# Performance work log

Measured on AMD Instinct MI355X. Metric: run time of the kernel, lower is better.

## Reference

```python
import jax, jax.numpy as jnp
import numpy as np

B, H, W, C = 2, 128, 256, 64
NHEAD, K, HIDDEN = 2, 9, 256
HD = C // NHEAD


def _layer_norm(x, g, b, eps=1e-5):
    m = jnp.mean(x, -1, keepdims=True)
    v = jnp.mean((x - m) ** 2, -1, keepdims=True)
    return (x - m) * jax.lax.rsqrt(v + eps) * g + b


def _grid_sample(img, gx, gy):
    """Bilinear grid_sample, zeros padding, align_corners=False.
    img: (N, Ch, Hh, Ww); gx, gy: (N, P) normalized coords in [-1, 1].
    Returns (N, Ch, P)."""
    N, Ch, Hh, Ww = img.shape
    ix = (gx + 1.0) * (Ww * 0.5) - 0.5
    iy = (gy + 1.0) * (Hh * 0.5) - 0.5
    x0 = jnp.floor(ix)
    y0 = jnp.floor(iy)
    flat = img.reshape(N, Ch, Hh * Ww)

    def gather(xi, yi):
        valid = (xi >= 0) & (xi <= Ww - 1) & (yi >= 0) & (yi <= Hh - 1)
        xc = jnp.clip(xi, 0, Ww - 1).astype(jnp.int32)
        yc = jnp.clip(yi, 0, Hh - 1).astype(jnp.int32)
        vals = jnp.take_along_axis(flat, (yc * Ww + xc)[:, None, :], axis=2)
        return vals * valid[:, None, :].astype(img.dtype)

    wx1 = ix - x0
    wy1 = iy - y0
    return (gather(x0, y0) * ((1 - wx1) * (1 - wy1))[:, None, :]
            + gather(x0 + 1, y0) * (wx1 * (1 - wy1))[:, None, :]
            + gather(x0, y0 + 1) * ((1 - wx1) * wy1)[:, None, :]
            + gather(x0 + 1, y0 + 1) * (wx1 * wy1)[:, None, :])


def setup_inputs() -> dict:
    key = jax.random.key(0)
    ks = jax.random.split(key, 16)
    s = 0.02
    inp = {}
    inp['x'] = jax.random.normal(ks[0], (B, H * W, C), jnp.float32)
    # spherical-style reference points: 3x3 pixel neighborhood per query, normalized coords
    ys = (np.arange(H) + 0.5) / H * 2 - 1
    xs = (np.arange(W) + 0.5) / W * 2 - 1
    gy, gx = np.meshgrid(ys, xs, indexing='ij')
    dy, dx = np.meshgrid(np.array([-1, 0, 1]), np.array([-1, 0, 1]), indexing='ij')
    offs = np.stack([dx.ravel() * 2.0 / W, dy.ravel() * 2.0 / H], -1)  # (9,2) in (x,y)
    ref = np.stack([gx, gy], -1)[:, :, None, :] + offs[None, None]     # (H,W,9,2)
    inp['ref_point'] = jnp.asarray(np.broadcast_to(ref, (B, H, W, K, 2)).copy(), jnp.float32)
    # norm1 / norm2
    inp['g1'] = jnp.ones((C,), jnp.float32); inp['be1'] = jnp.zeros((C,), jnp.float32)
    inp['g2'] = jnp.ones((C,), jnp.float32); inp['be2'] = jnp.zeros((C,), jnp.float32)
    # deformable attention projections
    inp['Woff'] = jax.random.normal(ks[1], (C, NHEAD * K * 2), jnp.float32) * s
    inp['boff'] = jnp.zeros((NHEAD * K * 2,), jnp.float32)
    inp['Wa'] = jax.random.normal(ks[2], (C, NHEAD * K), jnp.float32) * s
    inp['ba'] = jnp.zeros((NHEAD * K,), jnp.float32)
    inp['Wv'] = jax.random.normal(ks[3], (C, C), jnp.float32) * s
    inp['bv'] = jnp.zeros((C,), jnp.float32)
    inp['Wo'] = jax.random.normal(ks[4], (C, C), jnp.float32) * s
    inp['bo'] = jnp.zeros((C,), jnp.float32)
    # LeFF
    inp['W1'] = jax.random.normal(ks[5], (C, HIDDEN), jnp.float32) * s
    inp['c1'] = jnp.zeros((HIDDEN,), jnp.float32)
    inp['Wdw'] = jax.random.normal(ks[6], (HIDDEN, 1, 3, 3), jnp.float32) * s
    inp['bdw'] = jnp.zeros((HIDDEN,), jnp.float32)
    inp['W2'] = jax.random.normal(ks[7], (HIDDEN, C), jnp.float32) * s
    inp['c2'] = jnp.zeros((C,), jnp.float32)
    return inp


def reference(x, ref_point, g1, be1, g2, be2, Woff, boff, Wa, ba, Wv, bv, Wo, bo,
              W1, c1, Wdw, bdw, W2, c2):
    # ---- norm1 + deformable k=9 point-sampling self-attention ----
    h = _layer_norm(x, g1, be1).reshape(B, H, W, C)
    off = (h @ Woff + boff).reshape(B, H, W, NHEAD, K, 2)
    attn = jax.nn.softmax((h @ Wa + ba).reshape(B, H, W, NHEAD, K), axis=-1)
    v = (h @ Wv + bv).reshape(B, H, W, NHEAD, HD)
    v = v.transpose(0, 3, 4, 1, 2).reshape(B * NHEAD, HD, H, W)
    loc = ref_point[:, :, :, None] + off                     # (B,H,W,NHEAD,K,2)
    loc = loc.transpose(0, 3, 1, 2, 4, 5).reshape(B * NHEAD, H * W * K, 2)
    samp = _grid_sample(v, loc[..., 0], loc[..., 1])          # (B*NHEAD, HD, H*W*K)
    samp = samp.reshape(B, NHEAD, HD, H, W, K)
    out = jnp.einsum('bnchwk,bhwnk->bhwnc', samp, attn).reshape(B, H, W, C)
    out = (out @ Wo + bo).reshape(B, H * W, C)
    x = x + out                                               # residual
    # ---- norm2 + LeFF (linear -> circular-pad depthwise 3x3 -> linear) ----
    y = _layer_norm(x, g2, be2)
    y = jax.nn.gelu(y @ W1 + c1, approximate=False)
    y = y.reshape(B, H, W, HIDDEN).transpose(0, 3, 1, 2)      # (B,HIDDEN,H,W)
    y = jnp.pad(y, ((0, 0), (0, 0), (0, 0), (1, 1)), mode='wrap')   # circular in width
    y = jnp.pad(y, ((0, 0), (0, 0), (1, 1), (0, 0)))                # zeros in height
    y = jax.lax.conv_general_dilated(y, Wdw, (1, 1), 'VALID',
                                     dimension_numbers=('NCHW', 'OIHW', 'NCHW'),
                                     feature_group_count=HIDDEN)
    y = jax.nn.gelu(y + bdw[None, :, None, None], approximate=False)
    y = y.transpose(0, 2, 3, 1).reshape(B, H * W, HIDDEN)
    y = y @ W2 + c2
    return x + y
```

## Files before the change

kernel.cpp:

```cpp
#include <hip/hip_runtime.h>
#include <math.h>

#define Bq 2
#define Hq 128
#define Wq 256
#define Cq 64
#define HIDq 256
#define HWq (Hq * Wq)
#define NTOK (Bq * HWq)

#define TOKA 64
#define TOKB 64
#define TOKC 64
#define PIXD 32

typedef __attribute__((ext_vector_type(8))) short short8v;
typedef __attribute__((ext_vector_type(4))) float f32x4v;
typedef __attribute__((ext_vector_type(4))) unsigned short ushort4v;
typedef __attribute__((ext_vector_type(4))) unsigned int uint4v;

__device__ inline float gelu_exact(float x) {
    return 0.5f * x * (1.0f + erff(x * 0.70710678118654752440f));
}

__device__ inline unsigned short f2bf(float f) {
    unsigned int u = __float_as_uint(f);
    u += 0x7FFFu + ((u >> 16) & 1u);
    return (unsigned short)(u >> 16);
}

__device__ inline float bf2f(unsigned short u) {
    return __uint_as_float(((unsigned int)u) << 16);
}

__global__ __launch_bounds__(256) void kPrep(
    const float* __restrict__ W1, const float* __restrict__ W2,
    const float* __restrict__ Wv, const float* __restrict__ Woff, const float* __restrict__ Wa,
    unsigned short* __restrict__ w1t, unsigned short* __restrict__ w2t,
    unsigned short* __restrict__ wct)
{
    const int p = blockIdx.x * 256 + threadIdx.x;
    if (p < 8192) {
        const int c = p >> 5, k2 = p & 31;
        const unsigned int pk = (unsigned int)f2bf(W1[(size_t)(2 * k2) * 256 + c])
                              | ((unsigned int)f2bf(W1[(size_t)(2 * k2 + 1) * 256 + c]) << 16);
        ((unsigned int*)w1t)[c * 32 + k2] = pk;
    } else if (p < 16384) {
        const int q = p - 8192;
        const int c = q >> 7, k2 = q & 127;
        const unsigned int pk = (unsigned int)f2bf(W2[(size_t)(2 * k2) * 64 + c])
                              | ((unsigned int)f2bf(W2[(size_t)(2 * k2 + 1) * 64 + c]) << 16);
        ((unsigned int*)w2t)[c * 128 + k2] = pk;
    } else {
        const int q = p - 16384;
        const int c = q >> 5, k2 = q & 31;
        float w0 = 0.0f, w1 = 0.0f;
        if (c < 64)       { w0 = Wv[(size_t)(2 * k2) * 64 + c];          w1 = Wv[(size_t)(2 * k2 + 1) * 64 + c]; }
        else if (c < 100) { w0 = Woff[(size_t)(2 * k2) * 36 + (c - 64)]; w1 = Woff[(size_t)(2 * k2 + 1) * 36 + (c - 64)]; }
        else if (c < 118) { w0 = Wa[(size_t)(2 * k2) * 18 + (c - 100)];  w1 = Wa[(size_t)(2 * k2 + 1) * 18 + (c - 100)]; }
        const unsigned int pk = (unsigned int)f2bf(w0) | ((unsigned int)f2bf(w1) << 16);
        ((unsigned int*)wct)[c * 32 + k2] = pk;
    }
}

__device__ inline void ln_to_bf16_lds(
    const float* __restrict__ xsrc, const float* __restrict__ g, const float* __restrict__ be,
    int tok0, int t, unsigned short* __restrict__ hdst)
{
    const int tok = t >> 2, part = t & 3;
    const int chb = part * 16;
    const float* xp = xsrc + (size_t)(tok0 + tok) * 64 + chb;
    const float4 v0 = ((const float4*)xp)[0];
    const float4 v1 = ((const float4*)xp)[1];
    const float4 v2 = ((const float4*)xp)[2];
    const float4 v3 = ((const float4*)xp)[3];
    float s = ((v0.x + v0.y) + (v0.z + v0.w)) + ((v1.x + v1.y) + (v1.z + v1.w))
            + ((v2.x + v2.y) + (v2.z + v2.w)) + ((v3.x + v3.y) + (v3.z + v3.w));
    float s2 = 0.0f;
    s2 = fmaf(v0.x, v0.x, s2); s2 = fmaf(v0.y, v0.y, s2);
    s2 = fmaf(v0.z, v0.z, s2); s2 = fmaf(v0.w, v0.w, s2);
    s2 = fmaf(v1.x, v1.x, s2); s2 = fmaf(v1.y, v1.y, s2);
    s2 = fmaf(v1.z, v1.z, s2); s2 = fmaf(v1.w, v1.w, s2);
    s2 = fmaf(v2.x, v2.x, s2); s2 = fmaf(v2.y, v2.y, s2);
    s2 = fmaf(v2.z, v2.z, s2); s2 = fmaf(v2.w, v2.w, s2);
    s2 = fmaf(v3.x, v3.x, s2); s2 = fmaf(v3.y, v3.y, s2);
    s2 = fmaf(v3.z, v3.z, s2); s2 = fmaf(v3.w, v3.w, s2);
    s  += __shfl_xor(s, 1);  s2 += __shfl_xor(s2, 1);
    s  += __shfl_xor(s, 2);  s2 += __shfl_xor(s2, 2);
    const float m  = s * (1.0f / 64.0f);
    const float var = fmaf(-m, m, s2 * (1.0f / 64.0f));
    const float rs = rsqrtf(var + 1e-5f);
    const float nb = -m * rs;
    const float vv[16] = {v0.x,v0.y,v0.z,v0.w, v1.x,v1.y,v1.z,v1.w,
                          v2.x,v2.y,v2.z,v2.w, v3.x,v3.y,v3.z,v3.w};
    unsigned int pk[8];
    #pragma unroll
    for (int q = 0; q < 8; ++q) {
        const float hA = fmaf(fmaf(vv[2*q], rs, nb), g[chb + 2*q], be[chb + 2*q]);
        const float hB = fmaf(fmaf(vv[2*q+1], rs, nb), g[chb + 2*q+1], be[chb + 2*q+1]);
        pk[q] = (unsigned int)f2bf(hA) | ((unsigned int)f2bf(hB) << 16);
    }
    const unsigned int swz = ((unsigned int)(tok & 7)) << 3;
    unsigned int hi0 = ((unsigned int)(tok * 64 + chb)) ^ swz;
    unsigned int hi1 = ((unsigned int)(tok * 64 + chb + 8)) ^ swz;
    uint4 gA = {pk[0], pk[1], pk[2], pk[3]};
    uint4 gB = {pk[4], pk[5], pk[6], pk[7]};
    *(uint4*)&hdst[hi0] = gA;
    *(uint4*)&hdst[hi1] = gB;
}

__global__ __launch_bounds__(256) void kA(
    const float* __restrict__ x,
    const float* __restrict__ g1, const float* __restrict__ be1,
    const unsigned short* __restrict__ wct, const float* __restrict__ bv,
    unsigned char* __restrict__ v8)
{
    __shared__ unsigned short WvT[64 * 64];
    __shared__ unsigned short hb[TOKA * 64];
    __shared__ unsigned char vtile[TOKA * 64];
    const int t = threadIdx.x;
    const int tok0 = blockIdx.x * TOKA;
    const int b = tok0 >> 15;
    const int pix0 = tok0 & (HWq - 1);

    #pragma unroll
    for (int i = 0; i < 2; ++i) {
        const int q4 = t + i * 256;
        const uint4 d = ((const uint4*)wct)[q4];
        const int u0 = q4 * 4;
        const int c = u0 >> 5;
        const int udst = u0 ^ ((c & 7) << 2);
        *(uint4*)&((unsigned int*)WvT)[udst] = d;
    }
    ln_to_bf16_lds(x, g1, be1, tok0, t, hb);
    __syncthreads();

    const int lane = t & 63, wv = t >> 6;
    const int fr = lane & 15, kb = (lane >> 4) * 8;
    const int atok = wv * 16 + fr;
    f32x4v acc[4];
    #pragma unroll
    for (int nt = 0; nt < 4; ++nt) acc[nt] = (f32x4v){0.0f, 0.0f, 0.0f, 0.0f};
    #pragma unroll
    for (int ks = 0; ks < 2; ++ks) {
        const short8v a = *(const short8v*)&hb[(atok * 64 + ks * 32 + kb) ^ ((atok & 7) << 3)];
        #pragma unroll
        for (int nt = 0; nt < 4; ++nt) {
            const int col = nt * 16 + fr;
            const short8v bfr = *(const short8v*)&WvT[(col * 64 + ks * 32 + kb) ^ ((col & 7) << 3)];
            acc[nt] = __builtin_amdgcn_mfma_f32_16x16x32_bf16(a, bfr, acc[nt], 0, 0, 0);
        }
    }
    const int rbase = wv * 16 + (lane >> 4) * 4;
    #pragma unroll
    for (int nt = 0; nt < 4; ++nt) {
        const int col = nt * 16 + fr;
        const float bvv = bv[col];
        #pragma unroll
        for (int r = 0; r < 4; ++r) {
            const float val = acc[nt][r] + bvv;
            const int pk = __builtin_amdgcn_cvt_pk_fp8_f32(val, val, 0, false);
            vtile[(rbase + r) * 64 + col] = (unsigned char)(pk & 0xFF);
        }
    }
    __syncthreads();

    {
        const int tok = t >> 2, chunk = t & 3;
        const int n = chunk >> 1;
        const uint4 d = *(const uint4*)&vtile[tok * 64 + chunk * 16];
        *(uint4*)&v8[((size_t)(b * 2 + n) * HWq + pix0 + tok) * 32 + (chunk & 1) * 16] = d;
    }
}

__global__ __launch_bounds__(256) void kB(
    const float* __restrict__ x, const unsigned char* __restrict__ v8,
    const float* __restrict__ ref, const unsigned short* __restrict__ wct,
    const float* __restrict__ g1, const float* __restrict__ be1,
    const float* __restrict__ boff, const float* __restrict__ ba,
    const float* __restrict__ Wo, const float* __restrict__ bo,
    float* __restrict__ out)
{
    __shared__ float ldsf[9088];
    unsigned short* lds16 = (unsigned short*)ldsf;
    const int t = threadIdx.x;
    const int bid = (blockIdx.x & 7) * (NTOK / TOKB / 8) + (blockIdx.x >> 3);
    const int tok0 = bid * TOKB;
    const int b = tok0 >> 15;

    #pragma unroll
    for (int i = 0; i < 2; ++i) {
        const int q4 = t + i * 256;
        const uint4 d = ((const uint4*)wct)[q4 + 512];
        const int u0 = q4 * 4;
        const int c = u0 >> 5;
        const int udst = u0 ^ ((c & 7) << 2);
        *(uint4*)&((unsigned int*)lds16)[udst] = d;
    }
    ln_to_bf16_lds(x, g1, be1, tok0, t, lds16 + 4096);
    __syncthreads();

    const int lane = t & 63, wvid = t >> 6;
    {
        const int fr = lane & 15, kb = (lane >> 4) * 8;
        const int atok = wvid * 16 + fr;
        f32x4v acc[4];
        #pragma unroll
        for (int nt = 0; nt < 4; ++nt) acc[nt] = (f32x4v){0.0f, 0.0f, 0.0f, 0.0f};
        #pragma unroll
        for (int ks = 0; ks < 2; ++ks) {
            const short8v a = *(const short8v*)&lds16[4096 + ((atok * 64 + ks * 32 + kb) ^ ((atok & 7) << 3))];
            #pragma unroll
            for (int nt = 0; nt < 4; ++nt) {
                const int col = nt * 16 + fr;
                const short8v bfr = *(const short8v*)&lds16[(col * 64 + ks * 32 + kb) ^ ((col & 7) << 3)];
                acc[nt] = __builtin_amdgcn_mfma_f32_16x16x32_bf16(a, bfr, acc[nt], 0, 0, 0);
            }
        }
        const int rbase = wvid * 16 + (lane >> 4) * 4;
        #pragma unroll
        for (int nt = 0; nt < 4; ++nt) {
            const int col = nt * 16 + fr;
            if (col < 36) {
                const int rco = (col >= 18) ? col - 18 : col;
                const float bo_ = boff[col];
                #pragma unroll
                for (int r = 0; r < 4; ++r) {
                    const size_t tokg = (size_t)tok0 + rbase + r;
                    ldsf[4352 + (rbase + r) * 36 + col] = ref[tokg * 18 + rco] + acc[nt][r] + bo_;
                }
            } else if (col < 54) {
                const int lg = col - 36;
                const float bav = ba[lg];
                #pragma unroll
                for (int r = 0; r < 4; ++r) ldsf[7808 + (rbase + r) * 20 + lg] = acc[nt][r] + bav;
            }
        }
    }
    __syncthreads();

    if (t < TOKB * 2) {
        const int tk = t >> 1, head = t & 1;
        float mx = -1e30f;
        #pragma unroll
        for (int k = 0; k < 9; ++k) mx = fmaxf(mx, ldsf[7808 + tk * 20 + head * 9 + k]);
        float e[9], s = 0.0f;
        #pragma unroll
        for (int k = 0; k < 9; ++k) { e[k] = expf(ldsf[7808 + tk * 20 + head * 9 + k] - mx); s += e[k]; }
        const float inv = 1.0f / s;
        #pragma unroll
        for (int k = 0; k < 9; ++k) ldsf[6656 + tk * 18 + head * 9 + k] = e[k] * inv;
    }
    __syncthreads();

    {
        const int half = lane & 1;
        const int n = (lane >> 1) & 1;
        const int tkl = wvid * 16 + (lane >> 2);
        const unsigned char* __restrict__ vimg =
            v8 + (size_t)(b * 2 + n) * HWq * 32 + half * 16;

        float a[16];
        #pragma unroll
        for (int j = 0; j < 16; ++j) a[j] = 0.0f;

        #pragma unroll
        for (int k = 0; k < 9; ++k) {
            const float2 g = *(const float2*)&ldsf[4352 + tkl * 36 + n * 18 + 2 * k];
            const float at = ldsf[6656 + tkl * 18 + n * 9 + k];
            const float ix = fmaf(g.x, 128.0f, 127.5f);
            const float iy = fmaf(g.y, 64.0f, 63.5f);
            const float x0f = floorf(ix), y0f = floorf(iy);
            const float wx1 = ix - x0f, wy1 = iy - y0f;
            const float wx0 = 1.0f - wx1, wy0 = 1.0f - wy1;
            const int x0 = (int)x0f, y0 = (int)y0f;
            const int x1i = x0 + 1, y1i = y0 + 1;
            const int x0c = min(max(x0, 0), Wq - 1), y0c = min(max(y0, 0), Hq - 1);
            const int x1c = min(max(x1i, 0), Wq - 1), y1c = min(max(y1i, 0), Hq - 1);
            const bool vx0 = (x0 >= 0) & (x0 <= Wq - 1);
            const bool vy0 = (y0 >= 0) & (y0 <= Hq - 1);
            const bool vx1 = (x1i >= 0) & (x1i <= Wq - 1);
            const bool vy1 = (y1i >= 0) & (y1i <= Hq - 1);
            const float ax0 = at * wx0, ax1 = at * wx1;
            const float w00 = (vx0 && vy0) ? ax0 * wy0 : 0.0f;
            const float w10 = (vx1 && vy0) ? ax1 * wy0 : 0.0f;
            const float w01 = (vx0 && vy1) ? ax0 * wy1 : 0.0f;
            const float w11 = (vx1 && vy1) ? ax1 * wy1 : 0.0f;
            const int p00 = (((y0c << 8) + x0c) << 5), p10 = (((y0c << 8) + x1c) << 5);
            const int p01 = (((y1c << 8) + x0c) << 5), p11 = (((y1c << 8) + x1c) << 5);
            const uint4v q00 = *(const uint4v*)(vimg + p00);
            const uint4v q10 = *(const uint4v*)(vimg + p10);
            const uint4v q01 = *(const uint4v*)(vimg + p01);
            const uint4v q11 = *(const uint4v*)(vimg + p11);
            #pragma unroll
            for (int j = 0; j < 4; ++j) {
                {
                    auto lo = __builtin_amdgcn_cvt_pk_f32_fp8(q00[j], false);
                    auto hi = __builtin_amdgcn_cvt_pk_f32_fp8(q00[j], true);
                    a[4*j+0] = fmaf(w00, lo[0], a[4*j+0]); a[4*j+1] = fmaf(w00, lo[1], a[4*j+1]);
                    a[4*j+2] = fmaf(w00, hi[0], a[4*j+2]); a[4*j+3] = fmaf(w00, hi[1], a[4*j+3]);
                }
                {
                    auto lo = __builtin_amdgcn_cvt_pk_f32_fp8(q10[j], false);
                    auto hi = __builtin_amdgcn_cvt_pk_f32_fp8(q10[j], true);
                    a[4*j+0] = fmaf(w10, lo[0], a[4*j+0]); a[4*j+1] = fmaf(w10, lo[1], a[4*j+1]);
                    a[4*j+2] = fmaf(w10, hi[0], a[4*j+2]); a[4*j+3] = fmaf(w10, hi[1], a[4*j+3]);
                }
                {
                    auto lo = __builtin_amdgcn_cvt_pk_f32_fp8(q01[j], false);
                    auto hi = __builtin_amdgcn_cvt_pk_f32_fp8(q01[j], true);
                    a[4*j+0] = fmaf(w01, lo[0], a[4*j+0]); a[4*j+1] = fmaf(w01, lo[1], a[4*j+1]);
                    a[4*j+2] = fmaf(w01, hi[0], a[4*j+2]); a[4*j+3] = fmaf(w01, hi[1], a[4*j+3]);
                }
                {
                    auto lo = __builtin_amdgcn_cvt_pk_f32_fp8(q11[j], false);
                    auto hi = __builtin_amdgcn_cvt_pk_f32_fp8(q11[j], true);
                    a[4*j+0] = fmaf(w11, lo[0], a[4*j+0]); a[4*j+1] = fmaf(w11, lo[1], a[4*j+1]);
                    a[4*j+2] = fmaf(w11, hi[0], a[4*j+2]); a[4*j+3] = fmaf(w11, hi[1], a[4*j+3]);
                }
            }
        }
        const int ch0 = n * 32 + half * 16;
        float4 o0 = {a[0], a[1], a[2], a[3]};
        float4 o1 = {a[4], a[5], a[6], a[7]};
        float4 o2 = {a[8], a[9], a[10], a[11]};
        float4 o3 = {a[12], a[13], a[14], a[15]};
        *(float4*)&ldsf[tkl * 68 + ch0 + 0]  = o0;
        *(float4*)&ldsf[tkl * 68 + ch0 + 4]  = o1;
        *(float4*)&ldsf[tkl * 68 + ch0 + 8]  = o2;
        *(float4*)&ldsf[tkl * 68 + ch0 + 12] = o3;
    }
    __syncthreads();

    const int tg = t >> 3, cg8 = t & 7;
    const int tb = tg * 2, cb = cg8 * 8;
    float accw[2][8];
    #pragma unroll
    for (int i = 0; i < 2; ++i)
        #pragma unroll
        for (int q = 0; q < 8; ++q) accw[i][q] = 0.0f;

    for (int j = 0; j < 64; j += 4) {
        const float4 h0 = *(const float4*)&ldsf[(tb + 0) * 68 + j];
        const float4 h1 = *(const float4*)&ldsf[(tb + 1) * 68 + j];
        const float hv[2][4] = {{h0.x,h0.y,h0.z,h0.w},{h1.x,h1.y,h1.z,h1.w}};
        #pragma unroll
        for (int jj = 0; jj < 4; ++jj) {
            const float4 wA = *(const float4*)&Wo[(size_t)(j + jj) * 64 + cb];
            const float4 wB = *(const float4*)&Wo[(size_t)(j + jj) * 64 + cb + 4];
            const float wv8[8] = {wA.x,wA.y,wA.z,wA.w,wB.x,wB.y,wB.z,wB.w};
            #pragma unroll
            for (int i = 0; i < 2; ++i)
                #pragma unroll
                for (int q = 0; q < 8; ++q)
                    accw[i][q] = fmaf(hv[i][jj], wv8[q], accw[i][q]);
        }
    }
    const float4 boA = *(const float4*)&bo[cb];
    const float4 boB = *(const float4*)&bo[cb + 4];
    #pragma unroll
    for (int i = 0; i < 2; ++i) {
        const size_t tokg = (size_t)tok0 + tb + i;
        const float4 rA = *(const float4*)&x[tokg * 64 + cb];
        const float4 rB = *(const float4*)&x[tokg * 64 + cb + 4];
        float4 oA = {accw[i][0]+boA.x+rA.x, accw[i][1]+boA.y+rA.y,
                     accw[i][2]+boA.z+rA.z, accw[i][3]+boA.w+rA.w};
        float4 oB = {accw[i][4]+boB.x+rB.x, accw[i][5]+boB.y+rB.y,
                     accw[i][6]+boB.z+rB.z, accw[i][7]+boB.w+rB.w};
        *(float4*)&out[tokg * 64 + cb] = oA;
        *(float4*)&out[tokg * 64 + cb + 4] = oB;
    }
}

__global__ __launch_bounds__(512) void kC(
    const float* __restrict__ x1, const float* __restrict__ g2, const float* __restrict__ be2,
    const unsigned short* __restrict__ w1t, const float* __restrict__ c1,
    unsigned char* __restrict__ y8)
{
    __shared__ unsigned short W1T[256 * 64];
    __shared__ unsigned short hb2[TOKC * 64];
    __shared__ unsigned char ytile8[TOKC * 256];
    const int t = threadIdx.x;
    const int tok0 = blockIdx.x * TOKC;

    #pragma unroll
    for (int i = 0; i < 4; ++i) {
        const int q4 = t + i * 512;
        const uint4 d = ((const uint4*)w1t)[q4];
        const int u0 = q4 * 4;
        const int c = u0 >> 5;
        const int udst = u0 ^ ((c & 7) << 2);
        *(uint4*)&((unsigned int*)W1T)[udst] = d;
    }
    if (t < TOKC * 4) ln_to_bf16_lds(x1, g2, be2, tok0, t, hb2);
    __syncthreads();

    const int lane = t & 63, wv = t >> 6;
    const int mtile = wv & 3, nquad = wv >> 2;
    const int fr = lane & 15, kb = (lane >> 4) * 8;
    const int atok = mtile * 16 + fr;
    f32x4v acc[8];
    #pragma unroll
    for (int nt = 0; nt < 8; ++nt) acc[nt] = (f32x4v){0.0f, 0.0f, 0.0f, 0.0f};

    #pragma unroll
    for (int ks = 0; ks < 2; ++ks) {
        const short8v a = *(const short8v*)&hb2[(atok * 64 + ks * 32 + kb) ^ ((atok & 7) << 3)];
        #pragma unroll
        for (int nt = 0; nt < 8; ++nt) {
            const int col = nquad * 128 + nt * 16 + fr;
            const short8v bfr = *(const short8v*)&W1T[(col * 64 + ks * 32 + kb) ^ ((col & 7) << 3)];
            acc[nt] = __builtin_amdgcn_mfma_f32_16x16x32_bf16(a, bfr, acc[nt], 0, 0, 0);
        }
    }

    #pragma unroll
    for (int nt = 0; nt < 8; ++nt) {
        const int col = nquad * 128 + nt * 16 + fr;
        const float c1v = c1[col];
        #pragma unroll
        for (int r = 0; r < 4; ++r) {
            const int tok = mtile * 16 + (lane >> 4) * 4 + r;
            const float val = gelu_exact(acc[nt][r] + c1v);
            const int pk = __builtin_amdgcn_cvt_pk_fp8_f32(val, val, 0, false);
            ytile8[((unsigned)(tok * 256 + col)) ^ (((unsigned)(tok & 7)) << 4)] = (unsigned char)(pk & 0xFF);
        }
    }
    __syncthreads();

    {
        const int row = t >> 3, cb = (t & 7) * 32;
        const unsigned int swz = ((unsigned int)(row & 7)) << 4;
        unsigned char* dst = y8 + (size_t)(tok0 + row) * 256 + cb;
        #pragma unroll
        for (int j = 0; j < 2; ++j) {
            const unsigned int bidx = ((unsigned int)(row * 256 + cb + j * 16)) ^ swz;
            *(uint4*)(dst + j * 16) = *(const uint4*)&ytile8[bidx];
        }
    }
}

__global__ __launch_bounds__(256) void kD(
    const unsigned char* __restrict__ y8, const float* __restrict__ Wdw, const float* __restrict__ bdw,
    const unsigned short* __restrict__ w2t, const float* __restrict__ c2,
    float* __restrict__ out)
{
    __shared__ unsigned short zsb2[PIXD * 256];
    const int t = threadIdx.x;
    const int bid = (blockIdx.x & 7) * 256 + (blockIdx.x >> 3);
    const int b = bid >> 10;
    const int rem = bid & 1023;
    const int hh = rem >> 3;
    const int ww0 = (rem & 7) * PIXD;

    {
        const int lane = t & 63, sub = t >> 6;
        const int c4 = lane * 4;
        const int px0 = ww0 + sub * 8;
        const unsigned char* __restrict__ yb = y8 + (size_t)b * HWq * 256;
        const bool r0ok = (hh > 0), r2ok = (hh < Hq - 1);
        const int y0r = (hh - 1) << 8, y1r = hh << 8, y2r = (hh + 1) << 8;

        float um1[3][4], uz0[3][4], up1[3][4];
        #define LOADCOL(dst, xx) do {                                              \
            const unsigned int u0v = r0ok ? *(const unsigned int*)&yb[((size_t)(y0r + (xx)) << 8) + c4] : 0u; \
            const unsigned int u1v =        *(const unsigned int*)&yb[((size_t)(y1r + (xx)) << 8) + c4]; \
            const unsigned int u2v = r2ok ? *(const unsigned int*)&yb[((size_t)(y2r + (xx)) << 8) + c4] : 0u; \
            { auto lo = __builtin_amdgcn_cvt_pk_f32_fp8(u0v, false);               \
              auto hi = __builtin_amdgcn_cvt_pk_f32_fp8(u0v, true);                \
              dst[0][0] = lo[0]; dst[0][1] = lo[1]; dst[0][2] = hi[0]; dst[0][3] = hi[1]; } \
            { auto lo = __builtin_amdgcn_cvt_pk_f32_fp8(u1v, false);               \
              auto hi = __builtin_amdgcn_cvt_pk_f32_fp8(u1v, true);                \
              dst[1][0] = lo[0]; dst[1][1] = lo[1]; dst[1][2] = hi[0]; dst[1][3] = hi[1]; } \
            { auto lo = __builtin_amdgcn_cvt_pk_f32_fp8(u2v, false);               \
              auto hi = __builtin_amdgcn_cvt_pk_f32_fp8(u2v, true);                \
              dst[2][0] = lo[0]; dst[2][1] = lo[1]; dst[2][2] = hi[0]; dst[2][3] = hi[1]; } \
        } while (0)

        float wd[9][4], bdv[4];
        #pragma unroll
        for (int j = 0; j < 4; ++j) {
            bdv[j] = bdw[c4 + j];
            #pragma unroll
            for (int q = 0; q < 9; ++q) wd[q][j] = Wdw[(c4 + j) * 9 + q];
        }

        LOADCOL(um1, (px0 - 1) & 255);
        LOADCOL(uz0, px0);
        #pragma unroll
        for (int p = 0; p < 8; ++p) {
            LOADCOL(up1, (px0 + p + 1) & 255);
            unsigned short zq[4];
            #pragma unroll
            for (int j = 0; j < 4; ++j) {
                float a = bdv[j];
                #pragma unroll
                for (int ky = 0; ky < 3; ++ky) {
                    a = fmaf(wd[ky * 3 + 0][j], um1[ky][j], a);
                    a = fmaf(wd[ky * 3 + 1][j], uz0[ky][j], a);
                    a = fmaf(wd[ky * 3 + 2][j], up1[ky][j], a);
                }
                zq[j] = f2bf(gelu_exact(a));
            }
            const int pix = sub * 8 + p;
            ushort4v zv = {zq[0], zq[1], zq[2], zq[3]};
            *(ushort4v*)&zsb2[((unsigned)(pix * 256 + c4)) ^ (((unsigned)(pix & 7)) << 3)] = zv;
            #pragma unroll
            for (int ky = 0; ky < 3; ++ky)
                #pragma unroll
                for (int j = 0; j < 4; ++j) { um1[ky][j] = uz0[ky][j]; uz0[ky][j] = up1[ky][j]; }
        }
        #undef LOADCOL
    }
    __syncthreads();

    const int lane = t & 63, wv = t >> 6;
    const int fr = lane & 15;
    const int kb = (lane >> 4) * 8;
    const int col = wv * 16 + fr;
    f32x4v acc0 = {0.0f, 0.0f, 0.0f, 0.0f};
    f32x4v acc1 = {0.0f, 0.0f, 0.0f, 0.0f};
    #pragma unroll
    for (int kk = 0; kk < 8; ++kk) {
        const int ka = kk * 32 + kb;
        const short8v bfr = *(const short8v*)&w2t[(size_t)col * 256 + ka];
        const short8v a0 = *(const short8v*)&zsb2[(fr * 256 + ka) ^ ((fr & 7) << 3)];
        const short8v a1 = *(const short8v*)&zsb2[((fr + 16) * 256 + ka) ^ ((fr & 7) << 3)];
        acc0 = __builtin_amdgcn_mfma_f32_16x16x32_bf16(a0, bfr, acc0, 0, 0, 0);
        acc1 = __builtin_amdgcn_mfma_f32_16x16x32_bf16(a1, bfr, acc1, 0, 0, 0);
    }
    const float c2v = c2[col];
    #pragma unroll
    for (int r = 0; r < 4; ++r) {
        const int prow = (lane >> 4) * 4 + r;
        const size_t tok0g = (size_t)b * HWq + ((size_t)hh << 8) + ww0;
        out[(tok0g + prow) * 64 + col] += acc0[r] + c2v;
        out[(tok0g + 16 + prow) * 64 + col] += acc1[r] + c2v;
    }
}

extern "C" void kernel_launch(void* const* d_in, const int* in_sizes, int n_in,
                              void* d_out, int out_size, void* d_ws, size_t ws_size,
                              hipStream_t stream) {
    const float* x    = (const float*)d_in[0];
    const float* ref  = (const float*)d_in[1];
    const float* g1   = (const float*)d_in[2];
    const float* be1  = (const float*)d_in[3];
    const float* g2   = (const float*)d_in[4];
    const float* be2  = (const float*)d_in[5];
    const float* Woff = (const float*)d_in[6];
    const float* boff = (const float*)d_in[7];
    const float* Wa   = (const float*)d_in[8];
    const float* ba   = (const float*)d_in[9];
    const float* Wv   = (const float*)d_in[10];
    const float* bv   = (const float*)d_in[11];
    const float* Wo   = (const float*)d_in[12];
    const float* bo   = (const float*)d_in[13];
    const float* W1   = (const float*)d_in[14];
    const float* c1   = (const float*)d_in[15];
    const float* Wdw  = (const float*)d_in[16];
    const float* bdw  = (const float*)d_in[17];
    const float* W2   = (const float*)d_in[18];
    const float* c2   = (const float*)d_in[19];

    float* out = (float*)d_out;
    unsigned char* wsb = (unsigned char*)d_ws;
    unsigned char* v8 = wsb;
    unsigned char* y8 = v8 + (size_t)Bq * 2 * HWq * 32;
    unsigned short* w1t = (unsigned short*)(y8 + (size_t)NTOK * 256);
    unsigned short* w2t = w1t + 256 * 64;
    unsigned short* wct = w2t + 64 * 256;

    hipLaunchKernelGGL(kPrep, dim3(80), dim3(256), 0, stream,
                       W1, W2, Wv, Woff, Wa, w1t, w2t, wct);
    hipLaunchKernelGGL(kA, dim3(NTOK / TOKA), dim3(256), 0, stream,
                       x, g1, be1, wct, bv, v8);
    hipLaunchKernelGGL(kB, dim3(NTOK / TOKB), dim3(256), 0, stream,
                       x, v8, ref, wct, g1, be1, boff, ba, Wo, bo, out);
    hipLaunchKernelGGL(kC, dim3(NTOK / TOKC), dim3(512), 0, stream,
                       out, g2, be2, w1t, c1, y8);
    hipLaunchKernelGGL(kD, dim3(Bq * Hq * (Wq / PIXD)), dim3(256), 0, stream,
                       y8, Wdw, bdw, w2t, c2, out);
}
```

Measured before the change: 99.30 us.

## Double kB block to 512 threads, splitting per-thread work in sampling and projection

The deformable-attention kernel now runs 512 threads per block instead of 256. Work per thread is halved in each phase: the MFMA offset/logit GEMM splits N tiles across wave pairs, each sampling thread handles 8 channels (8-byte fp8 loads) instead of 16, and the Wo projection handles one token per thread. The aim is more memory-level parallelism and latency hiding in the gather-heavy sampling phase. In exchange it issues smaller loads, recomputes the bilinear coordinates and weights in twice as many threads, and adds pressure on occupancy from the larger blocks.

```diff
diff --git a/kernel.cpp b/kernel.cpp
--- a/kernel.cpp
+++ b/kernel.cpp
@@ -173,7 +173,7 @@
     }
 }
 
-__global__ __launch_bounds__(256) void kB(
+__global__ __launch_bounds__(512) void kB(
     const float* __restrict__ x, const unsigned char* __restrict__ v8,
     const float* __restrict__ ref, const unsigned short* __restrict__ wct,
     const float* __restrict__ g1, const float* __restrict__ be1,
@@ -188,52 +188,52 @@
     const int tok0 = bid * TOKB;
     const int b = tok0 >> 15;
 
-    #pragma unroll
-    for (int i = 0; i < 2; ++i) {
-        const int q4 = t + i * 256;
+    {
+        const int q4 = t;
         const uint4 d = ((const uint4*)wct)[q4 + 512];
         const int u0 = q4 * 4;
         const int c = u0 >> 5;
         const int udst = u0 ^ ((c & 7) << 2);
         *(uint4*)&((unsigned int*)lds16)[udst] = d;
     }
-    ln_to_bf16_lds(x, g1, be1, tok0, t, lds16 + 4096);
+    if (t < TOKB * 4) ln_to_bf16_lds(x, g1, be1, tok0, t, lds16 + 4096);
     __syncthreads();
 
     const int lane = t & 63, wvid = t >> 6;
     {
+        const int mtile = wvid & 3, npair = wvid >> 2;
         const int fr = lane & 15, kb = (lane >> 4) * 8;
-        const int atok = wvid * 16 + fr;
-        f32x4v acc[4];
-        #pragma unroll
-        for (int nt = 0; nt < 4; ++nt) acc[nt] = (f32x4v){0.0f, 0.0f, 0.0f, 0.0f};
+        const int atok = mtile * 16 + fr;
+        f32x4v acc[2];
+        acc[0] = (f32x4v){0.0f, 0.0f, 0.0f, 0.0f};
+        acc[1] = (f32x4v){0.0f, 0.0f, 0.0f, 0.0f};
         #pragma unroll
         for (int ks = 0; ks < 2; ++ks) {
             const short8v a = *(const short8v*)&lds16[4096 + ((atok * 64 + ks * 32 + kb) ^ ((atok & 7) << 3))];
             #pragma unroll
-            for (int nt = 0; nt < 4; ++nt) {
-                const int col = nt * 16 + fr;
+            for (int i = 0; i < 2; ++i) {
+                const int col = (npair * 2 + i) * 16 + fr;
                 const short8v bfr = *(const short8v*)&lds16[(col * 64 + ks * 32 + kb) ^ ((col & 7) << 3)];
-                acc[nt] = __builtin_amdgcn_mfma_f32_16x16x32_bf16(a, bfr, acc[nt], 0, 0, 0);
+                acc[i] = __builtin_amdgcn_mfma_f32_16x16x32_bf16(a, bfr, acc[i], 0, 0, 0);
             }
         }
-        const int rbase = wvid * 16 + (lane >> 4) * 4;
-        #pragma unroll
-        for (int nt = 0; nt < 4; ++nt) {
-            const int col = nt * 16 + fr;
+        const int rbase = mtile * 16 + (lane >> 4) * 4;
+        #pragma unroll
+        for (int i = 0; i < 2; ++i) {
+            const int col = (npair * 2 + i) * 16 + fr;
             if (col < 36) {
                 const int rco = (col >= 18) ? col - 18 : col;
                 const float bo_ = boff[col];
                 #pragma unroll
                 for (int r = 0; r < 4; ++r) {
                     const size_t tokg = (size_t)tok0 + rbase + r;
-                    ldsf[4352 + (rbase + r) * 36 + col] = ref[tokg * 18 + rco] + acc[nt][r] + bo_;
+                    ldsf[4352 + (rbase + r) * 36 + col] = ref[tokg * 18 + rco] + acc[i][r] + bo_;
                 }
             } else if (col < 54) {
                 const int lg = col - 36;
                 const float bav = ba[lg];
                 #pragma unroll
-                for (int r = 0; r < 4; ++r) ldsf[7808 + (rbase + r) * 20 + lg] = acc[nt][r] + bav;
+                for (int r = 0; r < 4; ++r) ldsf[7808 + (rbase + r) * 20 + lg] = acc[i][r] + bav;
             }
         }
     }
@@ -254,15 +254,16 @@
     __syncthreads();
 
     {
-        const int half = lane & 1;
-        const int n = (lane >> 1) & 1;
-        const int tkl = wvid * 16 + (lane >> 2);
+        const int tkl = t >> 3;
+        const int unit = t & 7;
+        const int n = unit >> 2;
+        const int o = unit & 3;
         const unsigned char* __restrict__ vimg =
-            v8 + (size_t)(b * 2 + n) * HWq * 32 + half * 16;
-
-        float a[16];
-        #pragma unroll
-        for (int j = 0; j < 16; ++j) a[j] = 0.0f;
+            v8 + (size_t)(b * 2 + n) * HWq * 32 + o * 8;
+
+        float a[8];
+        #pragma unroll
+        for (int j = 0; j < 8; ++j) a[j] = 0.0f;
 
         #pragma unroll
         for (int k = 0; k < 9; ++k) {
@@ -288,88 +289,62 @@
             const float w11 = (vx1 && vy1) ? ax1 * wy1 : 0.0f;
             const int p00 = (((y0c << 8) + x0c) << 5), p10 = (((y0c << 8) + x1c) << 5);
             const int p01 = (((y1c << 8) + x0c) << 5), p11 = (((y1c << 8) + x1c) << 5);
-            const uint4v q00 = *(const uint4v*)(vimg + p00);
-            const uint4v q10 = *(const uint4v*)(vimg + p10);
-            const uint4v q01 = *(const uint4v*)(vimg + p01);
-            const uint4v q11 = *(const uint4v*)(vimg + p11);
-            #pragma unroll
-            for (int j = 0; j < 4; ++j) {
-                {
-                    auto lo = __builtin_amdgcn_cvt_pk_f32_fp8(q00[j], false);
-                    auto hi = __builtin_amdgcn_cvt_pk_f32_fp8(q00[j], true);
-                    a[4*j+0] = fmaf(w00, lo[0], a[4*j+0]); a[4*j+1] = fmaf(w00, lo[1], a[4*j+1]);
-                    a[4*j+2] = fmaf(w00, hi[0], a[4*j+2]); a[4*j+3] = fmaf(w00, hi[1], a[4*j+3]);
-                }
-                {
-                    auto lo = __builtin_amdgcn_cvt_pk_f32_fp8(q10[j], false);
-                    auto hi = __builtin_amdgcn_cvt_pk_f32_fp8(q10[j], true);
-                    a[4*j+0] = fmaf(w10, lo[0], a[4*j+0]); a[4*j+1] = fmaf(w10, lo[1], a[4*j+1]);
-                    a[4*j+2] = fmaf(w10, hi[0], a[4*j+2]); a[4*j+3] = fmaf(w10, hi[1], a[4*j+3]);
-                }
-                {
-                    auto lo = __builtin_amdgcn_cvt_pk_f32_fp8(q01[j], false);
-                    auto hi = __builtin_amdgcn_cvt_pk_f32_fp8(q01[j], true);
-                    a[4*j+0] = fmaf(w01, lo[0], a[4*j+0]); a[4*j+1] = fmaf(w01, lo[1], a[4*j+1]);
-                    a[4*j+2] = fmaf(w01, hi[0], a[4*j+2]); a[4*j+3] = fmaf(w01, hi[1], a[4*j+3]);
-                }
-                {
-                    auto lo = __builtin_amdgcn_cvt_pk_f32_fp8(q11[j], false);
-                    auto hi = __builtin_amdgcn_cvt_pk_f32_fp8(q11[j], true);
-                    a[4*j+0] = fmaf(w11, lo[0], a[4*j+0]); a[4*j+1] = fmaf(w11, lo[1], a[4*j+1]);
-                    a[4*j+2] = fmaf(w11, hi[0], a[4*j+2]); a[4*j+3] = fmaf(w11, hi[1], a[4*j+3]);
-                }
-            }
-        }
-        const int ch0 = n * 32 + half * 16;
-        float4 o0 = {a[0], a[1], a[2], a[3]};
-        float4 o1 = {a[4], a[5], a[6], a[7]};
-        float4 o2 = {a[8], a[9], a[10], a[11]};
-        float4 o3 = {a[12], a[13], a[14], a[15]};
-        *(float4*)&ldsf[tkl * 68 + ch0 + 0]  = o0;
-        *(float4*)&ldsf[tkl * 68 + ch0 + 4]  = o1;
-        *(float4*)&ldsf[tkl * 68 + ch0 + 8]  = o2;
-        *(float4*)&ldsf[tkl * 68 + ch0 + 12] = o3;
+            const uint2 q00 = *(const uint2*)(vimg + p00);
+            const uint2 q10 = *(const uint2*)(vimg + p10);
+            const uint2 q01 = *(const uint2*)(vimg + p01);
+            const uint2 q11 = *(const uint2*)(vimg + p11);
+            #define ACC8(qq, ww) do {                                           \
+                auto lo0 = __builtin_amdgcn_cvt_pk_f32_fp8((qq).x, false);      \
+                auto hi0 = __builtin_amdgcn_cvt_pk_f32_fp8((qq).x, true);       \
+                auto lo1 = __builtin_amdgcn_cvt_pk_f32_fp8((qq).y, false);      \
+                auto hi1 = __builtin_amdgcn_cvt_pk_f32_fp8((qq).y, true);       \
+                a[0] = fmaf(ww, lo0[0], a[0]); a[1] = fmaf(ww, lo0[1], a[1]);   \
+                a[2] = fmaf(ww, hi0[0], a[2]); a[3] = fmaf(ww, hi0[1], a[3]);   \
+                a[4] = fmaf(ww, lo1[0], a[4]); a[5] = fmaf(ww, lo1[1], a[5]);   \
+                a[6] = fmaf(ww, hi1[0], a[6]); a[7] = fmaf(ww, hi1[1], a[7]);   \
+            } while (0)
+            ACC8(q00, w00);
+            ACC8(q10, w10);
+            ACC8(q01, w01);
+            ACC8(q11, w11);
+            #undef ACC8
+        }
+        const int ch0 = n * 32 + o * 8;
+        float4 oA = {a[0], a[1], a[2], a[3]};
+        float4 oB = {a[4], a[5], a[6], a[7]};
+        *(float4*)&ldsf[tkl * 68 + ch0 + 0] = oA;
+        *(float4*)&ldsf[tkl * 68 + ch0 + 4] = oB;
     }
     __syncthreads();
 
     const int tg = t >> 3, cg8 = t & 7;
-    const int tb = tg * 2, cb = cg8 * 8;
-    float accw[2][8];
-    #pragma unroll
-    for (int i = 0; i < 2; ++i)
-        #pragma unroll
-        for (int q = 0; q < 8; ++q) accw[i][q] = 0.0f;
+    const int cb = cg8 * 8;
+    float accw[8];
+    #pragma unroll
+    for (int q = 0; q < 8; ++q) accw[q] = 0.0f;
 
     for (int j = 0; j < 64; j += 4) {
-        const float4 h0 = *(const float4*)&ldsf[(tb + 0) * 68 + j];
-        const float4 h1 = *(const float4*)&ldsf[(tb + 1) * 68 + j];
-        const float hv[2][4] = {{h0.x,h0.y,h0.z,h0.w},{h1.x,h1.y,h1.z,h1.w}};
+        const float4 h = *(const float4*)&ldsf[tg * 68 + j];
+        const float hv[4] = {h.x, h.y, h.z, h.w};
         #pragma unroll
         for (int jj = 0; jj < 4; ++jj) {
             const float4 wA = *(const float4*)&Wo[(size_t)(j + jj) * 64 + cb];
             const float4 wB = *(const float4*)&Wo[(size_t)(j + jj) * 64 + cb + 4];
-            const float wv8[8] = {wA.x,wA.y,wA.z,wA.w,wB.x,wB.y,wB.z,wB.w};
-            #pragma unroll
-            for (int i = 0; i < 2; ++i)
-                #pragma unroll
-                for (int q = 0; q < 8; ++q)
-                    accw[i][q] = fmaf(hv[i][jj], wv8[q], accw[i][q]);
+            accw[0] = fmaf(hv[jj], wA.x, accw[0]); accw[1] = fmaf(hv[jj], wA.y, accw[1]);
+            accw[2] = fmaf(hv[jj], wA.z, accw[2]); accw[3] = fmaf(hv[jj], wA.w, accw[3]);
+            accw[4] = fmaf(hv[jj], wB.x, accw[4]); accw[5] = fmaf(hv[jj], wB.y, accw[5]);
+            accw[6] = fmaf(hv[jj], wB.z, accw[6]); accw[7] = fmaf(hv[jj], wB.w, accw[7]);
         }
     }
     const float4 boA = *(const float4*)&bo[cb];
     const float4 boB = *(const float4*)&bo[cb + 4];
-    #pragma unroll
-    for (int i = 0; i < 2; ++i) {
-        const size_t tokg = (size_t)tok0 + tb + i;
-        const float4 rA = *(const float4*)&x[tokg * 64 + cb];
-        const float4 rB = *(const float4*)&x[tokg * 64 + cb + 4];
-        float4 oA = {accw[i][0]+boA.x+rA.x, accw[i][1]+boA.y+rA.y,
-                     accw[i][2]+boA.z+rA.z, accw[i][3]+boA.w+rA.w};
-        float4 oB = {accw[i][4]+boB.x+rB.x, accw[i][5]+boB.y+rB.y,
-                     accw[i][6]+boB.z+rB.z, accw[i][7]+boB.w+rB.w};
-        *(float4*)&out[tokg * 64 + cb] = oA;
-        *(float4*)&out[tokg * 64 + cb + 4] = oB;
-    }
+    const size_t tokg = (size_t)tok0 + tg;
+    const float4 rA = *(const float4*)&x[tokg * 64 + cb];
+    const float4 rB = *(const float4*)&x[tokg * 64 + cb + 4];
+    float4 oA = {accw[0]+boA.x+rA.x, accw[1]+boA.y+rA.y, accw[2]+boA.z+rA.z, accw[3]+boA.w+rA.w};
+    float4 oB = {accw[4]+boB.x+rB.x, accw[5]+boB.y+rB.y, accw[6]+boB.z+rB.z, accw[7]+boB.w+rB.w};
+    *(float4*)&out[tokg * 64 + cb] = oA;
+    *(float4*)&out[tokg * 64 + cb + 4] = oB;
 }
 
 __global__ __launch_bounds__(512) void kC(
@@ -575,7 +550,7 @@
                        W1, W2, Wv, Woff, Wa, w1t, w2t, wct);
     hipLaunchKernelGGL(kA, dim3(NTOK / TOKA), dim3(256), 0, stream,
                        x, g1, be1, wct, bv, v8);
-    hipLaunchKernelGGL(kB, dim3(NTOK / TOKB), dim3(256), 0, stream,
+    hipLaunchKernelGGL(kB, dim3(NTOK / TOKB), dim3(512), 0, stream,
                        x, v8, ref, wct, g1, be1, boff, ba, Wo, bo, out);
     hipLaunchKernelGGL(kC, dim3(NTOK / TOKC), dim3(512), 0, stream,
                        out, g2, be2, w1t, c1, y8);
```

After: 111.4 us. 1.12x slower.

## Double kB block size to 512 threads, splitting sampling taps and projection work

Applied to the files above, without the earlier changes.

Raises the kB deformable-attention kernel from 256 to 512 threads per block. The offset/attention MFMA is split across twice as many waves, each covering half the output columns. The bilinear sampling loop splits the 9 taps across two thread groups (one gets a padded dead tap) and combines them with a cross-lane shuffle. The output projection now uses one token per thread. The aim is more parallelism and memory-level concurrency to hide gather latency, at the cost of extra shuffles, a wasted tap slot and different occupancy.

```diff
diff --git a/kernel.cpp b/kernel.cpp
--- a/kernel.cpp
+++ b/kernel.cpp
@@ -173,7 +173,7 @@
     }
 }
 
-__global__ __launch_bounds__(256) void kB(
+__global__ __launch_bounds__(512) void kB(
     const float* __restrict__ x, const unsigned char* __restrict__ v8,
     const float* __restrict__ ref, const unsigned short* __restrict__ wct,
     const float* __restrict__ g1, const float* __restrict__ be1,
@@ -188,52 +188,52 @@
     const int tok0 = bid * TOKB;
     const int b = tok0 >> 15;
 
-    #pragma unroll
-    for (int i = 0; i < 2; ++i) {
-        const int q4 = t + i * 256;
+    {
+        const int q4 = t;
         const uint4 d = ((const uint4*)wct)[q4 + 512];
         const int u0 = q4 * 4;
         const int c = u0 >> 5;
         const int udst = u0 ^ ((c & 7) << 2);
         *(uint4*)&((unsigned int*)lds16)[udst] = d;
     }
-    ln_to_bf16_lds(x, g1, be1, tok0, t, lds16 + 4096);
+    if (t < TOKB * 4) ln_to_bf16_lds(x, g1, be1, tok0, t, lds16 + 4096);
     __syncthreads();
 
     const int lane = t & 63, wvid = t >> 6;
     {
+        const int mtile = wvid & 3, npair = wvid >> 2;
         const int fr = lane & 15, kb = (lane >> 4) * 8;
-        const int atok = wvid * 16 + fr;
-        f32x4v acc[4];
-        #pragma unroll
-        for (int nt = 0; nt < 4; ++nt) acc[nt] = (f32x4v){0.0f, 0.0f, 0.0f, 0.0f};
+        const int atok = mtile * 16 + fr;
+        f32x4v acc[2];
+        acc[0] = (f32x4v){0.0f, 0.0f, 0.0f, 0.0f};
+        acc[1] = (f32x4v){0.0f, 0.0f, 0.0f, 0.0f};
         #pragma unroll
         for (int ks = 0; ks < 2; ++ks) {
             const short8v a = *(const short8v*)&lds16[4096 + ((atok * 64 + ks * 32 + kb) ^ ((atok & 7) << 3))];
             #pragma unroll
-            for (int nt = 0; nt < 4; ++nt) {
-                const int col = nt * 16 + fr;
+            for (int i = 0; i < 2; ++i) {
+                const int col = (npair * 2 + i) * 16 + fr;
                 const short8v bfr = *(const short8v*)&lds16[(col * 64 + ks * 32 + kb) ^ ((col & 7) << 3)];
-                acc[nt] = __builtin_amdgcn_mfma_f32_16x16x32_bf16(a, bfr, acc[nt], 0, 0, 0);
+                acc[i] = __builtin_amdgcn_mfma_f32_16x16x32_bf16(a, bfr, acc[i], 0, 0, 0);
             }
         }
-        const int rbase = wvid * 16 + (lane >> 4) * 4;
-        #pragma unroll
-        for (int nt = 0; nt < 4; ++nt) {
-            const int col = nt * 16 + fr;
+        const int rbase = mtile * 16 + (lane >> 4) * 4;
+        #pragma unroll
+        for (int i = 0; i < 2; ++i) {
+            const int col = (npair * 2 + i) * 16 + fr;
             if (col < 36) {
                 const int rco = (col >= 18) ? col - 18 : col;
                 const float bo_ = boff[col];
                 #pragma unroll
                 for (int r = 0; r < 4; ++r) {
                     const size_t tokg = (size_t)tok0 + rbase + r;
-                    ldsf[4352 + (rbase + r) * 36 + col] = ref[tokg * 18 + rco] + acc[nt][r] + bo_;
+                    ldsf[4352 + (rbase + r) * 36 + col] = ref[tokg * 18 + rco] + acc[i][r] + bo_;
                 }
             } else if (col < 54) {
                 const int lg = col - 36;
                 const float bav = ba[lg];
                 #pragma unroll
-                for (int r = 0; r < 4; ++r) ldsf[7808 + (rbase + r) * 20 + lg] = acc[nt][r] + bav;
+                for (int r = 0; r < 4; ++r) ldsf[7808 + (rbase + r) * 20 + lg] = acc[i][r] + bav;
             }
         }
     }
@@ -254,9 +254,11 @@
     __syncthreads();
 
     {
-        const int half = lane & 1;
-        const int n = (lane >> 1) & 1;
-        const int tkl = wvid * 16 + (lane >> 2);
+        const int tkl = t >> 3;
+        const int unit = t & 7;
+        const int half = unit & 1;
+        const int n = (unit >> 1) & 1;
+        const int ks = unit >> 2;
         const unsigned char* __restrict__ vimg =
             v8 + (size_t)(b * 2 + n) * HWq * 32 + half * 16;
 
@@ -265,9 +267,12 @@
         for (int j = 0; j < 16; ++j) a[j] = 0.0f;
 
         #pragma unroll
-        for (int k = 0; k < 9; ++k) {
+        for (int kk = 0; kk < 5; ++kk) {
+            const int kraw = kk * 2 + ks;
+            const bool live = (kraw < 9);
+            const int k = live ? kraw : 8;
             const float2 g = *(const float2*)&ldsf[4352 + tkl * 36 + n * 18 + 2 * k];
-            const float at = ldsf[6656 + tkl * 18 + n * 9 + k];
+            const float at = live ? ldsf[6656 + tkl * 18 + n * 9 + k] : 0.0f;
             const float ix = fmaf(g.x, 128.0f, 127.5f);
             const float iy = fmaf(g.y, 64.0f, 63.5f);
             const float x0f = floorf(ix), y0f = floorf(iy);
@@ -320,56 +325,50 @@
                 }
             }
         }
-        const int ch0 = n * 32 + half * 16;
-        float4 o0 = {a[0], a[1], a[2], a[3]};
-        float4 o1 = {a[4], a[5], a[6], a[7]};
-        float4 o2 = {a[8], a[9], a[10], a[11]};
-        float4 o3 = {a[12], a[13], a[14], a[15]};
-        *(float4*)&ldsf[tkl * 68 + ch0 + 0]  = o0;
-        *(float4*)&ldsf[tkl * 68 + ch0 + 4]  = o1;
-        *(float4*)&ldsf[tkl * 68 + ch0 + 8]  = o2;
-        *(float4*)&ldsf[tkl * 68 + ch0 + 12] = o3;
+        #pragma unroll
+        for (int j = 0; j < 16; ++j) a[j] += __shfl_xor(a[j], 4);
+        if (ks == 0) {
+            const int ch0 = n * 32 + half * 16;
+            float4 o0 = {a[0], a[1], a[2], a[3]};
+            float4 o1 = {a[4], a[5], a[6], a[7]};
+            float4 o2 = {a[8], a[9], a[10], a[11]};
+            float4 o3 = {a[12], a[13], a[14], a[15]};
+            *(float4*)&ldsf[tkl * 68 + ch0 + 0]  = o0;
+            *(float4*)&ldsf[tkl * 68 + ch0 + 4]  = o1;
+            *(float4*)&ldsf[tkl * 68 + ch0 + 8]  = o2;
+            *(float4*)&ldsf[tkl * 68 + ch0 + 12] = o3;
+        }
     }
     __syncthreads();
 
     const int tg = t >> 3, cg8 = t & 7;
-    const int tb = tg * 2, cb = cg8 * 8;
-    float accw[2][8];
-    #pragma unroll
-    for (int i = 0; i < 2; ++i)
-        #pragma unroll
-        for (int q = 0; q < 8; ++q) accw[i][q] = 0.0f;
+    const int cb = cg8 * 8;
+    float accw[8];
+    #pragma unroll
+    for (int q = 0; q < 8; ++q) accw[q] = 0.0f;
 
     for (int j = 0; j < 64; j += 4) {
-        const float4 h0 = *(const float4*)&ldsf[(tb + 0) * 68 + j];
-        const float4 h1 = *(const float4*)&ldsf[(tb + 1) * 68 + j];
-        const float hv[2][4] = {{h0.x,h0.y,h0.z,h0.w},{h1.x,h1.y,h1.z,h1.w}};
+        const float4 h = *(const float4*)&ldsf[tg * 68 + j];
+        const float hv[4] = {h.x, h.y, h.z, h.w};
         #pragma unroll
         for (int jj = 0; jj < 4; ++jj) {
             const float4 wA = *(const float4*)&Wo[(size_t)(j + jj) * 64 + cb];
             const float4 wB = *(const float4*)&Wo[(size_t)(j + jj) * 64 + cb + 4];
-            const float wv8[8] = {wA.x,wA.y,wA.z,wA.w,wB.x,wB.y,wB.z,wB.w};
-            #pragma unroll
-            for (int i = 0; i < 2; ++i)
-                #pragma unroll
-                for (int q = 0; q < 8; ++q)
-                    accw[i][q] = fmaf(hv[i][jj], wv8[q], accw[i][q]);
+            accw[0] = fmaf(hv[jj], wA.x, accw[0]); accw[1] = fmaf(hv[jj], wA.y, accw[1]);
+            accw[2] = fmaf(hv[jj], wA.z, accw[2]); accw[3] = fmaf(hv[jj], wA.w, accw[3]);
+            accw[4] = fmaf(hv[jj], wB.x, accw[4]); accw[5] = fmaf(hv[jj], wB.y, accw[5]);
+            accw[6] = fmaf(hv[jj], wB.z, accw[6]); accw[7] = fmaf(hv[jj], wB.w, accw[7]);
         }
     }
     const float4 boA = *(const float4*)&bo[cb];
     const float4 boB = *(const float4*)&bo[cb + 4];
-    #pragma unroll
-    for (int i = 0; i < 2; ++i) {
-        const size_t tokg = (size_t)tok0 + tb + i;
-        const float4 rA = *(const float4*)&x[tokg * 64 + cb];
-        const float4 rB = *(const float4*)&x[tokg * 64 + cb + 4];
-        float4 oA = {accw[i][0]+boA.x+rA.x, accw[i][1]+boA.y+rA.y,
-                     accw[i][2]+boA.z+rA.z, accw[i][3]+boA.w+rA.w};
-        float4 oB = {accw[i][4]+boB.x+rB.x, accw[i][5]+boB.y+rB.y,
-                     accw[i][6]+boB.z+rB.z, accw[i][7]+boB.w+rB.w};
-        *(float4*)&out[tokg * 64 + cb] = oA;
-        *(float4*)&out[tokg * 64 + cb + 4] = oB;
-    }
+    const size_t tokg = (size_t)tok0 + tg;
+    const float4 rA = *(const float4*)&x[tokg * 64 + cb];
+    const float4 rB = *(const float4*)&x[tokg * 64 + cb + 4];
+    float4 oA = {accw[0]+boA.x+rA.x, accw[1]+boA.y+rA.y, accw[2]+boA.z+rA.z, accw[3]+boA.w+rA.w};
+    float4 oB = {accw[4]+boB.x+rB.x, accw[5]+boB.y+rB.y, accw[6]+boB.z+rB.z, accw[7]+boB.w+rB.w};
+    *(float4*)&out[tokg * 64 + cb] = oA;
+    *(float4*)&out[tokg * 64 + cb + 4] = oB;
 }
 
 __global__ __launch_bounds__(512) void kC(
@@ -575,7 +574,7 @@
                        W1, W2, Wv, Woff, Wa, w1t, w2t, wct);
     hipLaunchKernelGGL(kA, dim3(NTOK / TOKA), dim3(256), 0, stream,
                        x, g1, be1, wct, bv, v8);
-    hipLaunchKernelGGL(kB, dim3(NTOK / TOKB), dim3(256), 0, stream,
+    hipLaunchKernelGGL(kB, dim3(NTOK / TOKB), dim3(512), 0, stream,
                        x, v8, ref, wct, g1, be1, boff, ba, Wo, bo, out);
     hipLaunchKernelGGL(kC, dim3(NTOK / TOKC), dim3(512), 0, stream,
                        out, g2, be2, w1t, c1, y8);
```

New measurement: 121.7 us. 1.23x slower.
